# Kernel tuning notes

Hardware: AMD Instinct MI355X
Metric: run time of the kernel (lower is better)

The kernel has to match this reference:

```python
import jax, jax.numpy as jnp
import numpy as np

IN_DIM = 256
K = 64
NB = 64  # num_blocks
N = NB * K
BATCH = 4096
DT = 0.05
TAU_EPS = 1e-6


def setup_inputs() -> dict:
    key = jax.random.key(0)
    ks = jax.random.split(key, 10)
    def xavier(k_, shape, fan_in, fan_out):
        lim = np.sqrt(6.0 / (fan_in + fan_out))
        return jax.random.uniform(k_, shape, jnp.float32, -lim, lim)
    return {
        "y": jax.random.normal(ks[0], (BATCH, N), jnp.float32),
        "u_t": jax.random.normal(ks[1], (BATCH, IN_DIM), jnp.float32),
        "tau_raw": jnp.zeros((N,), jnp.float32),
        "W_in_w": xavier(ks[2], (K, IN_DIM), IN_DIM, K),
        "W_in_b": jnp.zeros((K,), jnp.float32),
        "W_fwd_w": xavier(ks[3], (NB - 1, K, K), K, K),
        "W_fwd_b": jnp.zeros((NB - 1, K), jnp.float32),
        "W_rec_w": xavier(ks[4], (NB, K, K), K, K),
        "W_rec_b": jnp.zeros((NB, K), jnp.float32),
        "E_l": xavier(ks[5], (NB, K, K), K, K),
        "E_l_r": xavier(ks[6], (NB, K, K), K, K),
    }


def reference(y, u_t, tau_raw, W_in_w, W_in_b, W_fwd_w, W_fwd_b, W_rec_w, W_rec_b, E_l, E_l_r):
    yb = y.reshape(-1, NB, K)  # [batch, B, k]
    tau = jax.nn.softplus(tau_raw).reshape(NB, K) + TAU_EPS  # [B, k]
    # input drive for block 0 (torch Linear: x @ W^T + b)
    net0 = jnp.tanh(u_t @ W_in_w.T + W_in_b)  # [batch, k]
    # forward coupling for blocks 1..B-1, batched over blocks
    prev = yb[:, :-1, :]  # [batch, B-1, k]
    net_fwd = jnp.tanh(jnp.einsum('bji,joi->bjo', prev, W_fwd_w) + W_fwd_b)
    net_out = jnp.concatenate([net0[:, None, :], net_fwd], axis=1)  # [batch, B, k]
    # recurrent coupling, all blocks
    net_rec = jnp.tanh(jnp.einsum('bji,joi->bjo', yb, W_rec_w) + W_rec_b)
    decay = 1.0 / tau + jnp.abs(net_out) + jnp.abs(net_rec)  # [batch, B, k]
    drive = jnp.einsum('joi,bji->bjo', E_l, net_out) + jnp.einsum('joi,bji->bjo', E_l_r, net_rec)
    y_new = (yb + DT * drive) / (1.0 + DT * decay)
    return y_new.reshape(-1, N)
```

## Files before the change

kernel.cpp:

```cpp
#include <hip/hip_runtime.h>


#define IN_DIM 256
#define K 64
#define NB 64
#define BATCH 4096
#define NTOT (NB * K)
#define DTC 0.05f
#define TAU_EPS 1e-6f
#define LDSTR 72

typedef __bf16 bf16;
typedef bf16 bf16x8 __attribute__((ext_vector_type(8)));
typedef bf16 bf16x4 __attribute__((ext_vector_type(4)));
typedef float f32x4 __attribute__((ext_vector_type(4)));

__device__ __forceinline__ float fast_tanh(float x) {
    float e = __expf(2.0f * x);
    return 1.0f - 2.0f * __builtin_amdgcn_rcpf(e + 1.0f);
}

__device__ __forceinline__ void stage64(bf16* __restrict__ dst,
                                        const float* __restrict__ src,
                                        int gstride, int tid) {
#pragma unroll
    for (int it = 0; it < 2; ++it) {
        int idx = it * 512 + tid;
        int r = idx >> 4;
        int c4 = idx & 15;
        float4 v = *(const float4*)(src + r * gstride + (c4 << 2));
        bf16x4 p = { (bf16)v.x, (bf16)v.y, (bf16)v.z, (bf16)v.w };
        *(bf16x4*)(dst + r * LDSTR + (c4 << 2)) = p;
    }
}

__device__ __forceinline__ void load_afrag(const float* __restrict__ rowp,
                                           bf16x8& f0, bf16x8& f1) {
    float4 a0 = *(const float4*)(rowp);
    float4 a1 = *(const float4*)(rowp + 4);
    float4 a2 = *(const float4*)(rowp + 32);
    float4 a3 = *(const float4*)(rowp + 36);
    f0 = (bf16x8){ (bf16)a0.x, (bf16)a0.y, (bf16)a0.z, (bf16)a0.w,
                   (bf16)a1.x, (bf16)a1.y, (bf16)a1.z, (bf16)a1.w };
    f1 = (bf16x8){ (bf16)a2.x, (bf16)a2.y, (bf16)a2.z, (bf16)a2.w,
                   (bf16)a3.x, (bf16)a3.y, (bf16)a3.z, (bf16)a3.w };
}

__global__ __launch_bounds__(512, 4)
void ltcn_kernel(const float* __restrict__ y, const float* __restrict__ u_t,
                 const float* __restrict__ tau_raw,
                 const float* __restrict__ W_in_w, const float* __restrict__ W_in_b,
                 const float* __restrict__ W_fwd_w, const float* __restrict__ W_fwd_b,
                 const float* __restrict__ W_rec_w, const float* __restrict__ W_rec_b,
                 const float* __restrict__ E_l, const float* __restrict__ E_l_r,
                 float* __restrict__ out) {
    __shared__ bf16 sWf [64 * LDSTR];
    __shared__ bf16 sWr [64 * LDSTR];
    __shared__ bf16 sEl [64 * LDSTR];
    __shared__ bf16 sElr[64 * LDSTR];
    __shared__ float sInvTau[64], sBf[64], sBr[64];

    const int tid  = threadIdx.x;
    const int j    = blockIdx.y;
    const int b0   = blockIdx.x * 128;
    const int wave = tid >> 6;
    const int lane = tid & 63;
    const int quad = lane >> 4;
    const int l16  = lane & 15;
    const int am   = wave * 16 + l16;

    stage64(sWr,  W_rec_w + (size_t)j * K * K, K, tid);
    stage64(sEl,  E_l     + (size_t)j * K * K, K, tid);
    stage64(sElr, E_l_r   + (size_t)j * K * K, K, tid);

    bf16x8 yc0, yc1;
    load_afrag(y + (size_t)(b0 + am) * NTOT + j * K + quad * 8, yc0, yc1);

    bf16x8 yp0, yp1;
    if (j != 0) {
        stage64(sWf, W_fwd_w + (size_t)(j - 1) * K * K, K, tid);
        load_afrag(y + (size_t)(b0 + am) * NTOT + (j - 1) * K + quad * 8, yp0, yp1);
    } else {
        stage64(sWf, W_in_w, IN_DIM, tid);
        load_afrag(u_t + (size_t)(b0 + am) * IN_DIM + quad * 8, yp0, yp1);
    }
    if (tid < 64) {
        float x = tau_raw[j * K + tid];
        float sp = (x > 15.0f) ? x : log1pf(__expf(x));
        sInvTau[tid] = 1.0f / (sp + TAU_EPS);
        sBf[tid] = (j == 0) ? W_in_b[tid] : W_fwd_b[(j - 1) * K + tid];
        sBr[tid] = W_rec_b[j * K + tid];
    }
    __syncthreads();

    f32x4 accF[4] = {}, accR[4] = {};
    const int boff = quad * 8;
#pragma unroll
    for (int ct = 0; ct < 4; ++ct) {
        const bf16* br = sWr + (ct * 16 + l16) * LDSTR + boff;
        accR[ct] = __builtin_amdgcn_mfma_f32_16x16x32_bf16(yc0, *(const bf16x8*)br,        accR[ct], 0, 0, 0);
        accR[ct] = __builtin_amdgcn_mfma_f32_16x16x32_bf16(yc1, *(const bf16x8*)(br + 32), accR[ct], 0, 0, 0);
    }
    if (j != 0) {
#pragma unroll
        for (int ct = 0; ct < 4; ++ct) {
            const bf16* bw = sWf + (ct * 16 + l16) * LDSTR + boff;
            accF[ct] = __builtin_amdgcn_mfma_f32_16x16x32_bf16(yp0, *(const bf16x8*)bw,        accF[ct], 0, 0, 0);
            accF[ct] = __builtin_amdgcn_mfma_f32_16x16x32_bf16(yp1, *(const bf16x8*)(bw + 32), accF[ct], 0, 0, 0);
        }
    } else {
#pragma unroll 1
        for (int kc = 0; kc < 4; ++kc) {
#pragma unroll
            for (int ct = 0; ct < 4; ++ct) {
                const bf16* bw = sWf + (ct * 16 + l16) * LDSTR + boff;
                accF[ct] = __builtin_amdgcn_mfma_f32_16x16x32_bf16(yp0, *(const bf16x8*)bw,        accF[ct], 0, 0, 0);
                accF[ct] = __builtin_amdgcn_mfma_f32_16x16x32_bf16(yp1, *(const bf16x8*)(bw + 32), accF[ct], 0, 0, 0);
            }
            if (kc < 3) {
                load_afrag(u_t + (size_t)(b0 + am) * IN_DIM + (kc + 1) * 64 + quad * 8, yp0, yp1);
                __syncthreads();
                stage64(sWf, W_in_w + (kc + 1) * 64, IN_DIM, tid);
                __syncthreads();
            }
        }
    }

    float absum[4][4];
#pragma unroll
    for (int ct = 0; ct < 4; ++ct) {
        float bfv = sBf[ct * 16 + l16];
        float brv = sBr[ct * 16 + l16];
        float itv = sInvTau[ct * 16 + l16];
#pragma unroll
        for (int r = 0; r < 4; ++r) {
            float no = fast_tanh(accF[ct][r] + bfv);
            float nr = fast_tanh(accR[ct][r] + brv);
            accF[ct][r] = no;
            accR[ct][r] = nr;
            absum[ct][r] = itv + fabsf(no) + fabsf(nr);
        }
    }
    __syncthreads();

    bf16* band = (wave < 4) ? (sWf + wave * 16 * LDSTR)
                            : (sWr + (wave - 4) * 16 * LDSTR);
    const bf16* ap = band + l16 * LDSTR + boff;

#pragma unroll
    for (int ct = 0; ct < 4; ++ct)
#pragma unroll
        for (int r = 0; r < 4; ++r)
            band[(quad * 4 + r) * LDSTR + ct * 16 + l16] = (bf16)accF[ct][r];

    bf16x8 aO0 = *(const bf16x8*)ap, aO1 = *(const bf16x8*)(ap + 32);

    f32x4 accD[4] = {};
#pragma unroll
    for (int ct = 0; ct < 4; ++ct) {
        const bf16* bo = sEl + (ct * 16 + l16) * LDSTR + boff;
        accD[ct] = __builtin_amdgcn_mfma_f32_16x16x32_bf16(aO0, *(const bf16x8*)bo,        accD[ct], 0, 0, 0);
        accD[ct] = __builtin_amdgcn_mfma_f32_16x16x32_bf16(aO1, *(const bf16x8*)(bo + 32), accD[ct], 0, 0, 0);
    }

#pragma unroll
    for (int ct = 0; ct < 4; ++ct)
#pragma unroll
        for (int r = 0; r < 4; ++r)
            band[(quad * 4 + r) * LDSTR + ct * 16 + l16] = (bf16)accR[ct][r];

    bf16x8 aR0 = *(const bf16x8*)ap, aR1 = *(const bf16x8*)(ap + 32);

    float ye[4][4];
    const float* yep = y + (size_t)(b0 + wave * 16 + quad * 4) * NTOT + (size_t)j * K + l16;
#pragma unroll
    for (int ct = 0; ct < 4; ++ct)
#pragma unroll
        for (int r = 0; r < 4; ++r)
            ye[ct][r] = yep[(size_t)r * NTOT + ct * 16];

#pragma unroll
    for (int ct = 0; ct < 4; ++ct) {
        const bf16* br = sElr + (ct * 16 + l16) * LDSTR + boff;
        accD[ct] = __builtin_amdgcn_mfma_f32_16x16x32_bf16(aR0, *(const bf16x8*)br,        accD[ct], 0, 0, 0);
        accD[ct] = __builtin_amdgcn_mfma_f32_16x16x32_bf16(aR1, *(const bf16x8*)(br + 32), accD[ct], 0, 0, 0);
    }

#pragma unroll
    for (int ct = 0; ct < 4; ++ct) {
#pragma unroll
        for (int r = 0; r < 4; ++r) {
            size_t gi = (size_t)(b0 + wave * 16 + quad * 4 + r) * NTOT + j * K + ct * 16 + l16;
            out[gi] = (ye[ct][r] + DTC * accD[ct][r])
                      * __builtin_amdgcn_rcpf(1.0f + DTC * absum[ct][r]);
        }
    }
}

extern "C" void kernel_launch(void* const* d_in, const int* in_sizes, int n_in,
                              void* d_out, int out_size, void* d_ws, size_t ws_size,
                              hipStream_t stream) {
    const float* y       = (const float*)d_in[0];
    const float* u_t     = (const float*)d_in[1];
    const float* tau_raw = (const float*)d_in[2];
    const float* W_in_w  = (const float*)d_in[3];
    const float* W_in_b  = (const float*)d_in[4];
    const float* W_fwd_w = (const float*)d_in[5];
    const float* W_fwd_b = (const float*)d_in[6];
    const float* W_rec_w = (const float*)d_in[7];
    const float* W_rec_b = (const float*)d_in[8];
    const float* E_l     = (const float*)d_in[9];
    const float* E_l_r   = (const float*)d_in[10];
    float* out = (float*)d_out;

    dim3 grid(BATCH / 128, NB);
    hipLaunchKernelGGL(ltcn_kernel, grid, dim3(512), 0, stream,
                       y, u_t, tau_raw, W_in_w, W_in_b, W_fwd_w, W_fwd_b,
                       W_rec_w, W_rec_b, E_l, E_l_r, out);
}
```

Measured before the change: 162.9 us.

## Prepack weights into MFMA fragment layout via separate kernel, drop LDS staging

Adds a pre-pass kernel that converts all weight matrices to bf16 in the exact per-lane MFMA B-fragment order and precomputes inverse tau into workspace. The main kernel then loads B fragments directly from global (L2-resident) memory instead of staging them through LDS with barriers, and uses separate LDS bands for the tanh outputs so barriers are removed. This cuts per-block staging work and synchronization, at the cost of an extra kernel launch and a larger vector-register footprint for the fragments.

```diff
diff --git a/kernel.cpp b/kernel.cpp
--- a/kernel.cpp
+++ b/kernel.cpp
@@ -9,29 +9,16 @@
 #define DTC 0.05f
 #define TAU_EPS 1e-6f
 #define LDSTR 72
+#define NMATS 259
+#define WS_W_OFF 16384
 
 typedef __bf16 bf16;
 typedef bf16 bf16x8 __attribute__((ext_vector_type(8)));
-typedef bf16 bf16x4 __attribute__((ext_vector_type(4)));
 typedef float f32x4 __attribute__((ext_vector_type(4)));
 
 __device__ __forceinline__ float fast_tanh(float x) {
     float e = __expf(2.0f * x);
     return 1.0f - 2.0f * __builtin_amdgcn_rcpf(e + 1.0f);
-}
-
-__device__ __forceinline__ void stage64(bf16* __restrict__ dst,
-                                        const float* __restrict__ src,
-                                        int gstride, int tid) {
-#pragma unroll
-    for (int it = 0; it < 2; ++it) {
-        int idx = it * 512 + tid;
-        int r = idx >> 4;
-        int c4 = idx & 15;
-        float4 v = *(const float4*)(src + r * gstride + (c4 << 2));
-        bf16x4 p = { (bf16)v.x, (bf16)v.y, (bf16)v.z, (bf16)v.w };
-        *(bf16x4*)(dst + r * LDSTR + (c4 << 2)) = p;
-    }
 }
 
 __device__ __forceinline__ void load_afrag(const float* __restrict__ rowp,
@@ -46,19 +33,51 @@
                    (bf16)a3.x, (bf16)a3.y, (bf16)a3.z, (bf16)a3.w };
 }
 
+__global__ __launch_bounds__(256)
+void pack_kernel(const float* __restrict__ W_in_w, const float* __restrict__ W_fwd_w,
+                 const float* __restrict__ W_rec_w, const float* __restrict__ E_l,
+                 const float* __restrict__ E_l_r, const float* __restrict__ tau_raw,
+                 void* __restrict__ ws) {
+    int gid = blockIdx.x * 256 + threadIdx.x;
+    float* invTau = (float*)ws;
+    bf16* pw = (bf16*)((char*)ws + WS_W_OFF);
+    if (gid < NMATS * 512) {
+        int m    = gid >> 9;
+        int r    = gid & 511;
+        int ct   = r >> 7;
+        int kh   = (r >> 6) & 1;
+        int lane = r & 63;
+        int n  = ct * 16 + (lane & 15);
+        int k0 = kh * 32 + (lane >> 4) * 8;
+        const float* src;
+        if      (m < 64)  src = W_rec_w + (size_t)m * 4096         + n * 64  + k0;
+        else if (m < 127) src = W_fwd_w + (size_t)(m - 64) * 4096  + n * 64  + k0;
+        else if (m < 191) src = E_l     + (size_t)(m - 127) * 4096 + n * 64  + k0;
+        else if (m < 255) src = E_l_r   + (size_t)(m - 191) * 4096 + n * 64  + k0;
+        else              src = W_in_w  + (size_t)n * IN_DIM + (m - 255) * 64 + k0;
+        float4 a = *(const float4*)src;
+        float4 b = *(const float4*)(src + 4);
+        bf16x8 o = { (bf16)a.x, (bf16)a.y, (bf16)a.z, (bf16)a.w,
+                     (bf16)b.x, (bf16)b.y, (bf16)b.z, (bf16)b.w };
+        *(bf16x8*)(pw + (size_t)gid * 8) = o;
+    } else if (gid < NMATS * 512 + NTOT) {
+        int i = gid - NMATS * 512;
+        float x = tau_raw[i];
+        float sp = (x > 15.0f) ? x : log1pf(__expf(x));
+        invTau[i] = 1.0f / (sp + TAU_EPS);
+    }
+}
+
 __global__ __launch_bounds__(512, 4)
-void ltcn_kernel(const float* __restrict__ y, const float* __restrict__ u_t,
-                 const float* __restrict__ tau_raw,
-                 const float* __restrict__ W_in_w, const float* __restrict__ W_in_b,
-                 const float* __restrict__ W_fwd_w, const float* __restrict__ W_fwd_b,
-                 const float* __restrict__ W_rec_w, const float* __restrict__ W_rec_b,
-                 const float* __restrict__ E_l, const float* __restrict__ E_l_r,
-                 float* __restrict__ out) {
-    __shared__ bf16 sWf [64 * LDSTR];
-    __shared__ bf16 sWr [64 * LDSTR];
-    __shared__ bf16 sEl [64 * LDSTR];
-    __shared__ bf16 sElr[64 * LDSTR];
-    __shared__ float sInvTau[64], sBf[64], sBr[64];
+void ltcn_main(const float* __restrict__ y, const float* __restrict__ u_t,
+               const float* __restrict__ W_in_b, const float* __restrict__ W_fwd_b,
+               const float* __restrict__ W_rec_b, const void* __restrict__ ws,
+               float* __restrict__ out) {
+    __shared__ bf16 sNo[128 * LDSTR];
+    __shared__ bf16 sNr[128 * LDSTR];
+
+    const float* invTau = (const float*)ws;
+    const bf16*  pw     = (const bf16*)((const char*)ws + WS_W_OFF);
 
     const int tid  = threadIdx.x;
     const int j    = blockIdx.y;
@@ -68,108 +87,124 @@
     const int quad = lane >> 4;
     const int l16  = lane & 15;
     const int am   = wave * 16 + l16;
-
-    stage64(sWr,  W_rec_w + (size_t)j * K * K, K, tid);
-    stage64(sEl,  E_l     + (size_t)j * K * K, K, tid);
-    stage64(sElr, E_l_r   + (size_t)j * K * K, K, tid);
-
-    bf16x8 yc0, yc1;
-    load_afrag(y + (size_t)(b0 + am) * NTOT + j * K + quad * 8, yc0, yc1);
-
-    bf16x8 yp0, yp1;
+    const int boff = quad * 8;
+
+    bf16x8 yc0, yc1, yp0, yp1;
+    load_afrag(y + (size_t)(b0 + am) * NTOT + j * K + boff, yc0, yc1);
+    if (j != 0) load_afrag(y + (size_t)(b0 + am) * NTOT + (j - 1) * K + boff, yp0, yp1);
+    else        load_afrag(u_t + (size_t)(b0 + am) * IN_DIM + boff, yp0, yp1);
+
+    float brv[4], bfv[4], itv[4];
+#pragma unroll
+    for (int ct = 0; ct < 4; ++ct) {
+        int n = ct * 16 + l16;
+        brv[ct] = W_rec_b[j * K + n];
+        itv[ct] = invTau[j * K + n];
+        bfv[ct] = (j == 0) ? W_in_b[n] : W_fwd_b[(j - 1) * K + n];
+    }
+
+    const bf16* mrec = pw + (size_t)j * 4096;
+    f32x4 accR[4] = {};
+    {
+        bf16x8 B0[4], B1[4];
+#pragma unroll
+        for (int ct = 0; ct < 4; ++ct) {
+            B0[ct] = *(const bf16x8*)(mrec + ((ct * 2 + 0) * 64 + lane) * 8);
+            B1[ct] = *(const bf16x8*)(mrec + ((ct * 2 + 1) * 64 + lane) * 8);
+        }
+#pragma unroll
+        for (int ct = 0; ct < 4; ++ct) {
+            accR[ct] = __builtin_amdgcn_mfma_f32_16x16x32_bf16(yc0, B0[ct], accR[ct], 0, 0, 0);
+            accR[ct] = __builtin_amdgcn_mfma_f32_16x16x32_bf16(yc1, B1[ct], accR[ct], 0, 0, 0);
+        }
+    }
+
+    f32x4 accF[4] = {};
     if (j != 0) {
-        stage64(sWf, W_fwd_w + (size_t)(j - 1) * K * K, K, tid);
-        load_afrag(y + (size_t)(b0 + am) * NTOT + (j - 1) * K + quad * 8, yp0, yp1);
-    } else {
-        stage64(sWf, W_in_w, IN_DIM, tid);
-        load_afrag(u_t + (size_t)(b0 + am) * IN_DIM + quad * 8, yp0, yp1);
-    }
-    if (tid < 64) {
-        float x = tau_raw[j * K + tid];
-        float sp = (x > 15.0f) ? x : log1pf(__expf(x));
-        sInvTau[tid] = 1.0f / (sp + TAU_EPS);
-        sBf[tid] = (j == 0) ? W_in_b[tid] : W_fwd_b[(j - 1) * K + tid];
-        sBr[tid] = W_rec_b[j * K + tid];
-    }
-    __syncthreads();
-
-    f32x4 accF[4] = {}, accR[4] = {};
-    const int boff = quad * 8;
-#pragma unroll
-    for (int ct = 0; ct < 4; ++ct) {
-        const bf16* br = sWr + (ct * 16 + l16) * LDSTR + boff;
-        accR[ct] = __builtin_amdgcn_mfma_f32_16x16x32_bf16(yc0, *(const bf16x8*)br,        accR[ct], 0, 0, 0);
-        accR[ct] = __builtin_amdgcn_mfma_f32_16x16x32_bf16(yc1, *(const bf16x8*)(br + 32), accR[ct], 0, 0, 0);
-    }
-    if (j != 0) {
-#pragma unroll
-        for (int ct = 0; ct < 4; ++ct) {
-            const bf16* bw = sWf + (ct * 16 + l16) * LDSTR + boff;
-            accF[ct] = __builtin_amdgcn_mfma_f32_16x16x32_bf16(yp0, *(const bf16x8*)bw,        accF[ct], 0, 0, 0);
-            accF[ct] = __builtin_amdgcn_mfma_f32_16x16x32_bf16(yp1, *(const bf16x8*)(bw + 32), accF[ct], 0, 0, 0);
+        const bf16* mfwd = pw + (size_t)(64 + j - 1) * 4096;
+        bf16x8 B0[4], B1[4];
+#pragma unroll
+        for (int ct = 0; ct < 4; ++ct) {
+            B0[ct] = *(const bf16x8*)(mfwd + ((ct * 2 + 0) * 64 + lane) * 8);
+            B1[ct] = *(const bf16x8*)(mfwd + ((ct * 2 + 1) * 64 + lane) * 8);
+        }
+#pragma unroll
+        for (int ct = 0; ct < 4; ++ct) {
+            accF[ct] = __builtin_amdgcn_mfma_f32_16x16x32_bf16(yp0, B0[ct], accF[ct], 0, 0, 0);
+            accF[ct] = __builtin_amdgcn_mfma_f32_16x16x32_bf16(yp1, B1[ct], accF[ct], 0, 0, 0);
         }
     } else {
 #pragma unroll 1
         for (int kc = 0; kc < 4; ++kc) {
+            if (kc) load_afrag(u_t + (size_t)(b0 + am) * IN_DIM + kc * 64 + boff, yp0, yp1);
+            const bf16* mwin = pw + (size_t)(255 + kc) * 4096;
+            bf16x8 B0[4], B1[4];
 #pragma unroll
             for (int ct = 0; ct < 4; ++ct) {
-                const bf16* bw = sWf + (ct * 16 + l16) * LDSTR + boff;
-                accF[ct] = __builtin_amdgcn_mfma_f32_16x16x32_bf16(yp0, *(const bf16x8*)bw,        accF[ct], 0, 0, 0);
-                accF[ct] = __builtin_amdgcn_mfma_f32_16x16x32_bf16(yp1, *(const bf16x8*)(bw + 32), accF[ct], 0, 0, 0);
+                B0[ct] = *(const bf16x8*)(mwin + ((ct * 2 + 0) * 64 + lane) * 8);
+                B1[ct] = *(const bf16x8*)(mwin + ((ct * 2 + 1) * 64 + lane) * 8);
             }
-            if (kc < 3) {
-                load_afrag(u_t + (size_t)(b0 + am) * IN_DIM + (kc + 1) * 64 + quad * 8, yp0, yp1);
-                __syncthreads();
-                stage64(sWf, W_in_w + (kc + 1) * 64, IN_DIM, tid);
-                __syncthreads();
+#pragma unroll
+            for (int ct = 0; ct < 4; ++ct) {
+                accF[ct] = __builtin_amdgcn_mfma_f32_16x16x32_bf16(yp0, B0[ct], accF[ct], 0, 0, 0);
+                accF[ct] = __builtin_amdgcn_mfma_f32_16x16x32_bf16(yp1, B1[ct], accF[ct], 0, 0, 0);
             }
         }
     }
 
+    const bf16* mel  = pw + (size_t)(127 + j) * 4096;
+    const bf16* melr = pw + (size_t)(191 + j) * 4096;
+    bf16x8 Bo0[4], Bo1[4];
+#pragma unroll
+    for (int ct = 0; ct < 4; ++ct) {
+        Bo0[ct] = *(const bf16x8*)(mel + ((ct * 2 + 0) * 64 + lane) * 8);
+        Bo1[ct] = *(const bf16x8*)(mel + ((ct * 2 + 1) * 64 + lane) * 8);
+    }
+
     float absum[4][4];
 #pragma unroll
     for (int ct = 0; ct < 4; ++ct) {
-        float bfv = sBf[ct * 16 + l16];
-        float brv = sBr[ct * 16 + l16];
-        float itv = sInvTau[ct * 16 + l16];
 #pragma unroll
         for (int r = 0; r < 4; ++r) {
-            float no = fast_tanh(accF[ct][r] + bfv);
-            float nr = fast_tanh(accR[ct][r] + brv);
+            float no = fast_tanh(accF[ct][r] + bfv[ct]);
+            float nr = fast_tanh(accR[ct][r] + brv[ct]);
             accF[ct][r] = no;
             accR[ct][r] = nr;
-            absum[ct][r] = itv + fabsf(no) + fabsf(nr);
-        }
-    }
-    __syncthreads();
-
-    bf16* band = (wave < 4) ? (sWf + wave * 16 * LDSTR)
-                            : (sWr + (wave - 4) * 16 * LDSTR);
-    const bf16* ap = band + l16 * LDSTR + boff;
-
-#pragma unroll
-    for (int ct = 0; ct < 4; ++ct)
-#pragma unroll
-        for (int r = 0; r < 4; ++r)
-            band[(quad * 4 + r) * LDSTR + ct * 16 + l16] = (bf16)accF[ct][r];
-
-    bf16x8 aO0 = *(const bf16x8*)ap, aO1 = *(const bf16x8*)(ap + 32);
+            absum[ct][r] = itv[ct] + fabsf(no) + fabsf(nr);
+        }
+    }
+
+    bf16* bandO = sNo + wave * 16 * LDSTR;
+    bf16* bandR = sNr + wave * 16 * LDSTR;
+#pragma unroll
+    for (int ct = 0; ct < 4; ++ct) {
+#pragma unroll
+        for (int r = 0; r < 4; ++r) {
+            int mrow = quad * 4 + r;
+            int n = ct * 16 + l16;
+            bandO[mrow * LDSTR + n] = (bf16)accF[ct][r];
+            bandR[mrow * LDSTR + n] = (bf16)accR[ct][r];
+        }
+    }
+
+    const bf16* apO = bandO + l16 * LDSTR + boff;
+    const bf16* apR = bandR + l16 * LDSTR + boff;
+    bf16x8 aO0 = *(const bf16x8*)apO, aO1 = *(const bf16x8*)(apO + 32);
+    bf16x8 aR0 = *(const bf16x8*)apR, aR1 = *(const bf16x8*)(apR + 32);
+
+    bf16x8 Be0[4], Be1[4];
+#pragma unroll
+    for (int ct = 0; ct < 4; ++ct) {
+        Be0[ct] = *(const bf16x8*)(melr + ((ct * 2 + 0) * 64 + lane) * 8);
+        Be1[ct] = *(const bf16x8*)(melr + ((ct * 2 + 1) * 64 + lane) * 8);
+    }
 
     f32x4 accD[4] = {};
 #pragma unroll
     for (int ct = 0; ct < 4; ++ct) {
-        const bf16* bo = sEl + (ct * 16 + l16) * LDSTR + boff;
-        accD[ct] = __builtin_amdgcn_mfma_f32_16x16x32_bf16(aO0, *(const bf16x8*)bo,        accD[ct], 0, 0, 0);
-        accD[ct] = __builtin_amdgcn_mfma_f32_16x16x32_bf16(aO1, *(const bf16x8*)(bo + 32), accD[ct], 0, 0, 0);
-    }
-
-#pragma unroll
-    for (int ct = 0; ct < 4; ++ct)
-#pragma unroll
-        for (int r = 0; r < 4; ++r)
-            band[(quad * 4 + r) * LDSTR + ct * 16 + l16] = (bf16)accR[ct][r];
-
-    bf16x8 aR0 = *(const bf16x8*)ap, aR1 = *(const bf16x8*)(ap + 32);
+        accD[ct] = __builtin_amdgcn_mfma_f32_16x16x32_bf16(aO0, Bo0[ct], accD[ct], 0, 0, 0);
+        accD[ct] = __builtin_amdgcn_mfma_f32_16x16x32_bf16(aO1, Bo1[ct], accD[ct], 0, 0, 0);
+    }
 
     float ye[4][4];
     const float* yep = y + (size_t)(b0 + wave * 16 + quad * 4) * NTOT + (size_t)j * K + l16;
@@ -181,9 +216,8 @@
 
 #pragma unroll
     for (int ct = 0; ct < 4; ++ct) {
-        const bf16* br = sElr + (ct * 16 + l16) * LDSTR + boff;
-        accD[ct] = __builtin_amdgcn_mfma_f32_16x16x32_bf16(aR0, *(const bf16x8*)br,        accD[ct], 0, 0, 0);
-        accD[ct] = __builtin_amdgcn_mfma_f32_16x16x32_bf16(aR1, *(const bf16x8*)(br + 32), accD[ct], 0, 0, 0);
+        accD[ct] = __builtin_amdgcn_mfma_f32_16x16x32_bf16(aR0, Be0[ct], accD[ct], 0, 0, 0);
+        accD[ct] = __builtin_amdgcn_mfma_f32_16x16x32_bf16(aR1, Be1[ct], accD[ct], 0, 0, 0);
     }
 
 #pragma unroll
@@ -213,8 +247,12 @@
     const float* E_l_r   = (const float*)d_in[10];
     float* out = (float*)d_out;
 
+    int pack_threads = NMATS * 512 + NTOT;
+    hipLaunchKernelGGL(pack_kernel, dim3((pack_threads + 255) / 256), dim3(256),
+                       0, stream,
+                       W_in_w, W_fwd_w, W_rec_w, E_l, E_l_r, tau_raw, d_ws);
+
     dim3 grid(BATCH / 128, NB);
-    hipLaunchKernelGGL(ltcn_kernel, grid, dim3(512), 0, stream,
-                       y, u_t, tau_raw, W_in_w, W_in_b, W_fwd_w, W_fwd_b,
-                       W_rec_w, W_rec_b, E_l, E_l_r, out);
-}
+    hipLaunchKernelGGL(ltcn_main, grid, dim3(512), 0, stream,
+                       y, u_t, W_in_b, W_fwd_b, W_rec_b, d_ws, out);
+}
```

Result: slower. 171.9 us (+5.5%).
